# Kernel tuning notes

Measured on AMD Instinct MI355X. Metric: run time of the kernel, lower is better.

The kernel has to match this reference:

```python
import jax, jax.numpy as jnp
import numpy as np

N_NODES = 50000
N_EDGES = 800000
NUM_GRAPHS = 256
BN_EPS = 1e-5


def setup_inputs() -> dict:
    key = jax.random.key(0)
    ks = jax.random.split(key, 16)
    in_dim, hid, out_dim = 64, 128, 1
    s = lambda k, shape, fan: jax.random.normal(k, shape, jnp.float32) / np.sqrt(fan)
    inp = {
        'x': jax.random.normal(ks[0], (N_NODES, in_dim), jnp.float32),
        'edge_index': jax.random.randint(ks[1], (2, N_EDGES), 0, N_NODES, jnp.int64),
        'batch': jnp.sort(jax.random.randint(ks[2], (N_NODES,), 0, NUM_GRAPHS, jnp.int64)),
        # SAGEConv layer 0 (in_dim->hid): Wn aggregated-neighbor weight (with bias), Wr root weight
        'Wn0': s(ks[3], (in_dim, hid), in_dim), 'Wr0': s(ks[4], (in_dim, hid), in_dim), 'b0': jnp.zeros((hid,), jnp.float32),
        'Wn1': s(ks[5], (hid, hid), hid), 'Wr1': s(ks[6], (hid, hid), hid), 'b1': jnp.zeros((hid,), jnp.float32),
        'Wn2': s(ks[7], (hid, hid), hid), 'Wr2': s(ks[8], (hid, hid), hid), 'b2': jnp.zeros((hid,), jnp.float32),
        'gamma': jnp.ones((3, hid), jnp.float32), 'beta': jnp.zeros((3, hid), jnp.float32),
        'fc1_W': s(ks[9], (hid, hid // 2), hid), 'fc1_b': jnp.zeros((hid // 2,), jnp.float32),
        'fc2_W': s(ks[10], (hid // 2, out_dim), hid // 2), 'fc2_b': jnp.zeros((out_dim,), jnp.float32),
    }
    return inp


def _sage_mean(x, src, dst, inv_deg, Wn, Wr, b):
    # mean-aggregate neighbor features then linear: lin_l(mean_j x_j) + lin_r(x_i)
    agg = jax.ops.segment_sum(x[src], dst, num_segments=N_NODES) * inv_deg
    return agg @ Wn + x @ Wr + b


def _bn_relu(h, g, bta):
    mu = jnp.mean(h, axis=0)
    var = jnp.var(h, axis=0)
    return jax.nn.relu((h - mu) * jax.lax.rsqrt(var + BN_EPS) * g + bta)


def reference(x, edge_index, batch, Wn0, Wr0, b0, Wn1, Wr1, b1, Wn2, Wr2, b2,
              gamma, beta, fc1_W, fc1_b, fc2_W, fc2_b):
    src, dst = edge_index[0], edge_index[1]
    deg = jax.ops.segment_sum(jnp.ones((src.shape[0],), x.dtype), dst, num_segments=N_NODES)
    inv_deg = (1.0 / jnp.maximum(deg, 1.0))[:, None]  # [N,1]

    h = _bn_relu(_sage_mean(x, src, dst, inv_deg, Wn0, Wr0, b0), gamma[0], beta[0])
    h = _bn_relu(_sage_mean(h, src, dst, inv_deg, Wn1, Wr1, b1), gamma[1], beta[1])
    h = _bn_relu(_sage_mean(h, src, dst, inv_deg, Wn2, Wr2, b2), gamma[2], beta[2])

    # global mean pool over graphs
    pooled = jax.ops.segment_sum(h, batch, num_segments=NUM_GRAPHS)
    cnt = jax.ops.segment_sum(jnp.ones((h.shape[0],), h.dtype), batch, num_segments=NUM_GRAPHS)
    pooled = pooled / jnp.maximum(cnt, 1.0)[:, None]

    z = jax.nn.relu(pooled @ fc1_W + fc1_b)
    return jax.nn.sigmoid(z @ fc2_W + fc2_b)  # [NUM_GRAPHS, 1]
```

## Files before the change

kernel.cpp:

```cpp
#include <hip/hip_runtime.h>

#define N_NODES 50000
#define N_EDGES 800000
#define NUM_GRAPHS 256
#define HID 128
#define IN_DIM 64
#define BN_EPS 1e-5f
#define SPREAD 16
#define NB 196
#define BUCKET 256
#define SCHUNK 4096
#define NCHUNK 196
#define PX_BLKS 1563
#define W0_BLKS 8
#define W1_BLKS 16
#define GB_BLKS 196

typedef __attribute__((ext_vector_type(8))) short bf16x8;
typedef __attribute__((ext_vector_type(4))) float f32x4;

__device__ __forceinline__ float bf2f(unsigned short u){ union{unsigned i;float f;}c; c.i=((unsigned)u)<<16; return c.f; }
__device__ __forceinline__ float bflo(unsigned w){ union{unsigned i;float f;}c; c.i=w<<16; return c.f; }
__device__ __forceinline__ float bfhi(unsigned w){ union{unsigned i;float f;}c; c.i=w&0xFFFF0000u; return c.f; }
__device__ __forceinline__ unsigned short f2bf(float f){ union{float f;unsigned i;}c; c.f=f; unsigned r=c.i+0x7FFF+((c.i>>16)&1); return (unsigned short)(r>>16); }
__device__ __forceinline__ unsigned fpack(float a, float b){
  union{float f;unsigned i;}ca,cb; ca.f=a; cb.f=b;
  unsigned ra=((ca.i+0x7FFF+((ca.i>>16)&1))>>16)&0xFFFFu;
  unsigned rb=(cb.i+0x7FFF+((cb.i>>16)&1))&0xFFFF0000u;
  return ra|rb;
}
__device__ __forceinline__ void acc8(float* a, uint4 u){
  a[0]+=bflo(u.x); a[1]+=bfhi(u.x); a[2]+=bflo(u.y); a[3]+=bfhi(u.y);
  a[4]+=bflo(u.z); a[5]+=bfhi(u.z); a[6]+=bflo(u.w); a[7]+=bfhi(u.w);
}

__global__ __launch_bounds__(256) void k_hist(const int* __restrict__ dst, int* __restrict__ bcount){
  __shared__ int h[NB];
  int t = threadIdx.x;
  for(int i=t;i<NB;i+=256) h[i]=0;
  __syncthreads();
  int base = blockIdx.x*SCHUNK;
  int n = min(SCHUNK, N_EDGES-base);
  for(int v=t; v<n; v+=256) atomicAdd(&h[dst[base+v]>>8], 1);
  __syncthreads();
  for(int i=t;i<NB;i+=256) if(h[i]) atomicAdd(&bcount[i], h[i]);
}

__global__ __launch_bounds__(256) void k_scatter_pack(const int* __restrict__ src, const int* __restrict__ dst,
      const int* __restrict__ bcount, int* __restrict__ bfill, unsigned* __restrict__ pairs,
      const float* __restrict__ x, unsigned short* __restrict__ H0,
      const float* __restrict__ Wn0, const float* __restrict__ Wr0, unsigned short* __restrict__ Bp0,
      const float* __restrict__ Wn1, const float* __restrict__ Wr1, unsigned short* __restrict__ Bp1,
      const float* __restrict__ Wn2, const float* __restrict__ Wr2, unsigned short* __restrict__ Bp2,
      const int* __restrict__ batch, int* __restrict__ gstart){
  __shared__ int h[NB], lbase[NB], gbase[NB], cur[NB];
  __shared__ int sc[256];
  __shared__ unsigned staged[SCHUNK];
  int blk = blockIdx.x, t = threadIdx.x;
  if(blk < NCHUNK){
    for(int i=t;i<NB;i+=256) h[i]=0;
    __syncthreads();
    int base = blk*SCHUNK;
    int n = min(SCHUNK, N_EDGES-base);
    for(int v=t; v<n; v+=256) atomicAdd(&h[dst[base+v]>>8], 1);
    __syncthreads();
    int bc = (t<NB)? bcount[t] : 0;
    sc[t]=bc; __syncthreads();
    for(int off=1;off<256;off<<=1){ int u=(t>=off)?sc[t-off]:0; __syncthreads(); sc[t]+=u; __syncthreads(); }
    int bb_t = sc[t]-bc;
    __syncthreads();
    int hv = (t<NB)? h[t] : 0;
    sc[t]=hv; __syncthreads();
    for(int off=1;off<256;off<<=1){ int u=(t>=off)?sc[t-off]:0; __syncthreads(); sc[t]+=u; __syncthreads(); }
    if(t<NB){ lbase[t]=sc[t]-hv; cur[t]=0; if(hv) gbase[t] = bb_t + atomicAdd(&bfill[t], hv); }
    __syncthreads();
    for(int v=t; v<n; v+=256){
      int s = src[base+v], d = dst[base+v];
      int b = d>>8;
      int rr = atomicAdd(&cur[b], 1);
      staged[lbase[b]+rr] = (unsigned)s | ((unsigned)(d&255)<<16) | ((unsigned)b<<24);
    }
    __syncthreads();
    for(int i=t; i<n; i+=256){
      unsigned p = staged[i];
      int b = (int)(p>>24);
      pairs[gbase[b] + (i - lbase[b])] = p;
    }
  } else if(blk < NCHUNK+PX_BLKS){
    int tid = (blk-NCHUNK)*256 + t;
    if(tid < N_NODES*8){
      int row = tid>>3, q = tid&7;
      float4 a = ((const float4*)x)[(size_t)row*16 + q*2];
      float4 b = ((const float4*)x)[(size_t)row*16 + q*2 + 1];
      uint4 o;
      o.x = fpack(a.x,a.y); o.y = fpack(a.z,a.w);
      o.z = fpack(b.x,b.y); o.w = fpack(b.z,b.w);
      ((uint4*)H0)[(size_t)row*8 + q] = o;
    }
  } else if(blk < NCHUNK+PX_BLKS+W0_BLKS+2*W1_BLKS){
    const float *Wn, *Wr; unsigned short* Bp; int KH, base;
    if(blk < NCHUNK+PX_BLKS+W0_BLKS){ Wn=Wn0; Wr=Wr0; Bp=Bp0; KH=IN_DIM; base=NCHUNK+PX_BLKS; }
    else if(blk < NCHUNK+PX_BLKS+W0_BLKS+W1_BLKS){ Wn=Wn1; Wr=Wr1; Bp=Bp1; KH=HID; base=NCHUNK+PX_BLKS+W0_BLKS; }
    else { Wn=Wn2; Wr=Wr2; Bp=Bp2; KH=HID; base=NCHUNK+PX_BLKS+W0_BLKS+W1_BLKS; }
    int NKS = (2*KH)/32;
    int id = (blk-base)*256 + t;
    if(id < 8*NKS*64){
      int lane = id & 63;
      int ks = (id>>6) % NKS;
      int nt = (id>>6) / NKS;
      int quad = lane>>4, m = lane&15;
      int c = nt*16 + m;
      unsigned short v[8];
      #pragma unroll
      for(int j=0;j<8;j++){
        int k = ks*32 + quad*8 + j;
        float w = (k < KH) ? Wn[(size_t)k*HID + c] : Wr[(size_t)(k-KH)*HID + c];
        v[j] = f2bf(w);
      }
      uint4 o;
      o.x = ((unsigned)v[1]<<16)|v[0]; o.y = ((unsigned)v[3]<<16)|v[2];
      o.z = ((unsigned)v[5]<<16)|v[4]; o.w = ((unsigned)v[7]<<16)|v[6];
      ((uint4*)Bp)[id] = o;
    }
  } else {
    int id = (blk - (NCHUNK+PX_BLKS+W0_BLKS+2*W1_BLKS))*256 + t;
    if(id < N_NODES){
      int b = batch[id];
      if(id == 0){
        for(int g=0; g<=b; g++) gstart[g] = 0;
      } else {
        int pv = batch[id-1];
        if(pv != b) for(int g=pv+1; g<=b; g++) gstart[g] = id;
      }
      if(id == N_NODES-1){
        for(int g=b+1; g<=NUM_GRAPHS; g++) gstart[g] = N_NODES;
      }
    }
  }
}

__global__ __launch_bounds__(1024) void k_csr(const unsigned* __restrict__ pairs, const int* __restrict__ bcount,
                int* __restrict__ rowptr, float* __restrict__ invdeg, unsigned short* __restrict__ eidx){
  __shared__ int cnt[BUCKET], cur[BUCKET], sc[BUCKET];
  __shared__ int bb[2];
  int t = threadIdx.x;
  int b = blockIdx.x;
  if(t==0){ bb[0]=0; bb[1]=0; }
  if(t<BUCKET) cnt[t]=0;
  __syncthreads();
  if(t<NB){
    int c = bcount[t];
    if(t<b)  atomicAdd(&bb[0], c);
    if(t<=b) atomicAdd(&bb[1], c);
  }
  __syncthreads();
  int e0 = bb[0], e1 = bb[1];
  int node0 = b*BUCKET;
  for(int i=e0+t; i<e1; i+=1024) atomicAdd(&cnt[(int)((pairs[i]>>16)&0xFF)], 1);
  __syncthreads();
  if(t<BUCKET) sc[t]=cnt[t];
  __syncthreads();
  for(int off=1;off<BUCKET;off<<=1){
    int u=0;
    if(t<BUCKET && t>=off) u=sc[t-off];
    __syncthreads();
    if(t<BUCKET) sc[t]+=u;
    __syncthreads();
  }
  if(t<BUCKET && node0+t < N_NODES){
    int pre = sc[t]-cnt[t] + e0;
    rowptr[node0+t] = pre;
    cur[t] = pre;
    invdeg[node0+t] = 1.0f/(float)max(cnt[t],1);
  }
  if(b==0 && t==0) rowptr[N_NODES] = N_EDGES;
  __syncthreads();
  for(int i=e0+t; i<e1; i+=1024){
    unsigned p = pairs[i];
    int pos = atomicAdd(&cur[(p>>16)&0xFF], 1);
    eidx[pos] = (unsigned short)(p & 0xFFFF);
  }
}

template<int KH>
__global__ __launch_bounds__(256) void k_agg_gemm(const unsigned short* __restrict__ H,
                     const unsigned short* __restrict__ eidx, const int* __restrict__ rowptr,
                     const float* __restrict__ invdeg,
                     const unsigned short* __restrict__ Bp, const float* __restrict__ bias,
                     unsigned short* __restrict__ raw,
                     float* __restrict__ psum, float* __restrict__ psq){
  const int NKS = (2*KH)/32;
  const int LKS = KH/32;
  const int F8  = KH/8;
  const int SPL = 16/F8;
  const int LDA = KH + 4;
  const int EDGE_CAP = 512;
  __shared__ unsigned short Alds[16*LDA];
  __shared__ unsigned short Elds[EDGE_CAP];
  __shared__ int rp[17];
  int t = threadIdx.x;
  int wave = t>>6, lane = t&63;
  int row0b = blockIdx.x*16;

  if(t < 17) rp[t] = rowptr[row0b + t];
  __syncthreads();
  int ebase = rp[0];
  int etot  = rp[16] - ebase;
  bool fits = (etot <= EDGE_CAP);
  if(fits){
    for(int i=t; i<etot; i+=256) Elds[i] = eidx[ebase + i];
  }
  __syncthreads();

  int rr = lane >> 4;
  int h  = (SPL==1) ? 0 : ((lane>>3)&1);
  int q  = lane & (F8-1);
  int li = wave*4 + rr;
  int b = rp[li] - ebase, e = rp[li+1] - ebase;
  float acc[8] = {0,0,0,0,0,0,0,0};

#define LDH(s) (*(const uint4*)(H + (size_t)(s)*KH + q*8))
#define GBODY(FETCH) { \
    int i = b + h; \
    for(; i + 7*SPL < e; i += 8*SPL){ \
      int s0=FETCH(i), s1=FETCH(i+SPL), s2=FETCH(i+2*SPL), s3=FETCH(i+3*SPL), \
          s4=FETCH(i+4*SPL), s5=FETCH(i+5*SPL), s6=FETCH(i+6*SPL), s7=FETCH(i+7*SPL); \
      uint4 u0=LDH(s0),u1=LDH(s1),u2=LDH(s2),u3=LDH(s3),u4=LDH(s4),u5=LDH(s5),u6=LDH(s6),u7=LDH(s7); \
      acc8(acc,u0); acc8(acc,u1); acc8(acc,u2); acc8(acc,u3); \
      acc8(acc,u4); acc8(acc,u5); acc8(acc,u6); acc8(acc,u7); \
    } \
    for(; i + 3*SPL < e; i += 4*SPL){ \
      int s0=FETCH(i), s1=FETCH(i+SPL), s2=FETCH(i+2*SPL), s3=FETCH(i+3*SPL); \
      uint4 u0=LDH(s0),u1=LDH(s1),u2=LDH(s2),u3=LDH(s3); \
      acc8(acc,u0); acc8(acc,u1); acc8(acc,u2); acc8(acc,u3); \
    } \
    for(; i < e; i += SPL){ \
      int s0=FETCH(i); uint4 u0=LDH(s0); acc8(acc,u0); \
    } }
#define FL(i) ((int)Elds[(i)])
#define FG(i) ((int)eidx[ebase + (i)])
  if(fits){ GBODY(FL) } else { GBODY(FG) }
#undef FL
#undef FG
#undef GBODY
#undef LDH

  if(SPL==2){
    #pragma unroll
    for(int k=0;k<8;k++) acc[k] += __shfl_xor(acc[k], 8, 64);
  }
  if(h==0){
    float id = invdeg[row0b + li];
    uint4 o;
    o.x = fpack(acc[0]*id, acc[1]*id); o.y = fpack(acc[2]*id, acc[3]*id);
    o.z = fpack(acc[4]*id, acc[5]*id); o.w = fpack(acc[6]*id, acc[7]*id);
    *(uint4*)(Alds + li*LDA + q*8) = o;
  }
  __syncthreads();

  int m = lane&15, quad = lane>>4;
  const unsigned short* Arow = Alds + m*LDA + quad*8;
  const unsigned short* Hrow = H + (size_t)(row0b+m)*KH + quad*8;
  f32x4 facc[2];
  facc[0] = (f32x4){0.f,0.f,0.f,0.f};
  facc[1] = (f32x4){0.f,0.f,0.f,0.f};
  #pragma unroll 1
  for(int ks=0; ks<NKS; ks++){
    bf16x8 a = (ks < LKS) ? *(const bf16x8*)(Arow + ks*32)
                          : *(const bf16x8*)(Hrow + (size_t)(ks-LKS)*32);
    const unsigned short* bp = Bp + (((size_t)(wave*2)*NKS + ks)*64 + lane)*8;
    bf16x8 b0 = *(const bf16x8*)(bp);
    bf16x8 b1 = *(const bf16x8*)(bp + (size_t)NKS*64*8);
    facc[0] = __builtin_amdgcn_mfma_f32_16x16x32_bf16(a, b0, facc[0], 0, 0, 0);
    facc[1] = __builtin_amdgcn_mfma_f32_16x16x32_bf16(a, b1, facc[1], 0, 0, 0);
  }
  int sp = blockIdx.x & (SPREAD-1);
  #pragma unroll
  for(int nt=0;nt<2;nt++){
    int col = wave*32 + nt*16 + m;
    float bv = bias[col];
    float s = 0.f, s2 = 0.f;
    #pragma unroll
    for(int reg=0;reg<4;reg++){
      float v = facc[nt][reg] + bv;
      int row = row0b + quad*4 + reg;
      raw[(size_t)row*HID + col] = f2bf(v);
      s += v; s2 += v*v;
    }
    s  += __shfl_xor(s, 16, 64);  s  += __shfl_xor(s, 32, 64);
    s2 += __shfl_xor(s2, 16, 64); s2 += __shfl_xor(s2, 32, 64);
    if(quad==0){
      atomicAdd(&psum[sp*HID+col], s);
      atomicAdd(&psq [sp*HID+col], s2);
    }
  }
}

__global__ __launch_bounds__(256) void k_transform(const unsigned short* __restrict__ raw,
      const float* __restrict__ psum, const float* __restrict__ psq,
      const float* __restrict__ gamma, const float* __restrict__ beta,
      unsigned short* __restrict__ Hout){
  __shared__ float s_sc[HID], s_sf[HID];
  int t = threadIdx.x;
  if(t < HID){
    float s=0.f, s2=0.f;
    #pragma unroll
    for(int i=0;i<SPREAD;i++){ s += psum[i*HID+t]; s2 += psq[i*HID+t]; }
    float mu  = s  * (1.0f/(float)N_NODES);
    float var = s2 * (1.0f/(float)N_NODES) - mu*mu;
    float rstd = rsqrtf(var + BN_EPS);
    float sc = rstd * gamma[t];
    s_sc[t] = sc; s_sf[t] = beta[t] - mu*sc;
  }
  __syncthreads();
  int tid = blockIdx.x*256 + t;
  if(tid >= N_NODES*16) return;
  int q = tid & 15;
  uint4 u = ((const uint4*)raw)[tid];
  float f0 = fmaxf(fmaf(bflo(u.x), s_sc[q*8+0], s_sf[q*8+0]), 0.f);
  float f1 = fmaxf(fmaf(bfhi(u.x), s_sc[q*8+1], s_sf[q*8+1]), 0.f);
  float f2 = fmaxf(fmaf(bflo(u.y), s_sc[q*8+2], s_sf[q*8+2]), 0.f);
  float f3 = fmaxf(fmaf(bfhi(u.y), s_sc[q*8+3], s_sf[q*8+3]), 0.f);
  float f4 = fmaxf(fmaf(bflo(u.z), s_sc[q*8+4], s_sf[q*8+4]), 0.f);
  float f5 = fmaxf(fmaf(bfhi(u.z), s_sc[q*8+5], s_sf[q*8+5]), 0.f);
  float f6 = fmaxf(fmaf(bflo(u.w), s_sc[q*8+6], s_sf[q*8+6]), 0.f);
  float f7 = fmaxf(fmaf(bfhi(u.w), s_sc[q*8+7], s_sf[q*8+7]), 0.f);
  uint4 o;
  o.x = fpack(f0,f1); o.y = fpack(f2,f3); o.z = fpack(f4,f5); o.w = fpack(f6,f7);
  ((uint4*)Hout)[tid] = o;
}

__global__ __launch_bounds__(256) void k_poolmlp(const unsigned short* __restrict__ raw,
      const int* __restrict__ gstart,
      const float* __restrict__ psum, const float* __restrict__ psq,
      const float* __restrict__ gamma, const float* __restrict__ beta,
      const float* __restrict__ fc1W, const float* __restrict__ fc1b,
      const float* __restrict__ fc2W, const float* __restrict__ fc2b,
      float* __restrict__ out){
  __shared__ float s_sc[HID], s_sf[HID];
  __shared__ float red[16][HID];
  __shared__ float p[HID];
  int g = blockIdx.x, t = threadIdx.x;
  if(t < HID){
    float s=0.f, s2=0.f;
    #pragma unroll
    for(int i=0;i<SPREAD;i++){ s += psum[i*HID+t]; s2 += psq[i*HID+t]; }
    float mu  = s  * (1.0f/(float)N_NODES);
    float var = s2 * (1.0f/(float)N_NODES) - mu*mu;
    float rstd = rsqrtf(var + BN_EPS);
    float sc = rstd * gamma[t];
    s_sc[t] = sc; s_sf[t] = beta[t] - mu*sc;
  }
  __syncthreads();
  int r0 = gstart[g], r1 = gstart[g+1];
  int q = t & 15, rr = t >> 4;
  float acc[8] = {0,0,0,0,0,0,0,0};
  for(int n = r0 + rr; n < r1; n += 16){
    uint4 u = ((const uint4*)raw)[(size_t)n*16 + q];
    acc[0] += fmaxf(fmaf(bflo(u.x), s_sc[q*8+0], s_sf[q*8+0]), 0.f);
    acc[1] += fmaxf(fmaf(bfhi(u.x), s_sc[q*8+1], s_sf[q*8+1]), 0.f);
    acc[2] += fmaxf(fmaf(bflo(u.y), s_sc[q*8+2], s_sf[q*8+2]), 0.f);
    acc[3] += fmaxf(fmaf(bfhi(u.y), s_sc[q*8+3], s_sf[q*8+3]), 0.f);
    acc[4] += fmaxf(fmaf(bflo(u.z), s_sc[q*8+4], s_sf[q*8+4]), 0.f);
    acc[5] += fmaxf(fmaf(bfhi(u.z), s_sc[q*8+5], s_sf[q*8+5]), 0.f);
    acc[6] += fmaxf(fmaf(bflo(u.w), s_sc[q*8+6], s_sf[q*8+6]), 0.f);
    acc[7] += fmaxf(fmaf(bfhi(u.w), s_sc[q*8+7], s_sf[q*8+7]), 0.f);
  }
  #pragma unroll
  for(int k=0;k<8;k++) red[rr][q*8+k] = acc[k];
  __syncthreads();
  if(t < HID){
    float s = 0.f;
    #pragma unroll
    for(int j=0;j<16;j++) s += red[j][t];
    float ic = 1.0f / fmaxf((float)(r1 - r0), 1.0f);
    p[t] = s * ic;
  }
  __syncthreads();
  if(t < 64){
    float z = fc1b[t];
    #pragma unroll 4
    for(int k=0;k<HID;k++) z += p[k]*fc1W[k*64 + t];
    z = fmaxf(z, 0.f);
    float v = z * fc2W[t];
    #pragma unroll
    for(int off=32; off>0; off>>=1) v += __shfl_down(v, off, 64);
    if(t==0) out[g] = 1.0f/(1.0f + expf(-(v + fc2b[0])));
  }
}

extern "C" void kernel_launch(void* const* d_in, const int* in_sizes, int n_in,
                              void* d_out, int out_size, void* d_ws, size_t ws_size,
                              hipStream_t stream){
  const float* x    = (const float*)d_in[0];
  const int*   ei   = (const int*)d_in[1];
  const int*   batch= (const int*)d_in[2];
  const float* Wn0=(const float*)d_in[3]; const float* Wr0=(const float*)d_in[4]; const float* b0=(const float*)d_in[5];
  const float* Wn1=(const float*)d_in[6]; const float* Wr1=(const float*)d_in[7]; const float* b1=(const float*)d_in[8];
  const float* Wn2=(const float*)d_in[9]; const float* Wr2=(const float*)d_in[10]; const float* b2=(const float*)d_in[11];
  const float* gamma=(const float*)d_in[12]; const float* beta=(const float*)d_in[13];
  const float* fc1W=(const float*)d_in[14]; const float* fc1b=(const float*)d_in[15];
  const float* fc2W=(const float*)d_in[16]; const float* fc2b=(const float*)d_in[17];
  float* out = (float*)d_out;

  char* ws = (char*)d_ws;
  size_t off = 0;
  auto alloc = [&](size_t bytes)->char*{ char* p = ws + off; off += (bytes + 255) & ~(size_t)255; return p; };

  char* zero0   = ws + off;
  int*   bcount = (int*)alloc((size_t)NB*4);
  int*   bfill  = (int*)alloc((size_t)NB*4);
  float* pstats = (float*)alloc((size_t)3*2*SPREAD*HID*4);
  size_t zbytes = (size_t)((ws + off) - zero0);

  unsigned short* H0  = (unsigned short*)alloc((size_t)N_NODES*IN_DIM*2);
  unsigned short* H1  = (unsigned short*)alloc((size_t)N_NODES*HID*2);
  unsigned short* H2  = (unsigned short*)alloc((size_t)N_NODES*HID*2);
  unsigned short* raw = (unsigned short*)alloc((size_t)N_NODES*HID*2);
  unsigned short* Bp0 = (unsigned short*)alloc((size_t)8*4*64*8*2);
  unsigned short* Bp1 = (unsigned short*)alloc((size_t)8*8*64*8*2);
  unsigned short* Bp2 = (unsigned short*)alloc((size_t)8*8*64*8*2);
  float* invdeg = (float*)alloc((size_t)N_NODES*4);
  int* rowptr   = (int*)alloc((size_t)(N_NODES+1)*4);
  unsigned short* eidx = (unsigned short*)alloc((size_t)N_EDGES*2);
  unsigned* pairs = (unsigned*)alloc((size_t)N_EDGES*4);
  int* gstart   = (int*)alloc((size_t)(NUM_GRAPHS+1)*4);

  auto psumL = [&](int l){ return pstats + (size_t)l*2*SPREAD*HID; };
  auto psqL  = [&](int l){ return pstats + (size_t)l*2*SPREAD*HID + (size_t)SPREAD*HID; };

  const int* src = ei;
  const int* dst = ei + N_EDGES;

  hipMemsetAsync(zero0, 0, zbytes, stream);

  k_hist<<<NCHUNK, 256, 0, stream>>>(dst, bcount);
  k_scatter_pack<<<NCHUNK+PX_BLKS+W0_BLKS+2*W1_BLKS+GB_BLKS, 256, 0, stream>>>(src, dst, bcount, bfill, pairs,
      x, H0, Wn0, Wr0, Bp0, Wn1, Wr1, Bp1, Wn2, Wr2, Bp2, batch, gstart);
  k_csr<<<NB, 1024, 0, stream>>>(pairs, bcount, rowptr, invdeg, eidx);

  const int AG_BLKS = (N_NODES + 15)/16;

  k_agg_gemm<IN_DIM><<<AG_BLKS, 256, 0, stream>>>(H0, eidx, rowptr, invdeg, Bp0, b0, raw, psumL(0), psqL(0));
  k_transform<<<(N_NODES*16)/256, 256, 0, stream>>>(raw, psumL(0), psqL(0), gamma+0*HID, beta+0*HID, H1);
  k_agg_gemm<HID><<<AG_BLKS, 256, 0, stream>>>(H1, eidx, rowptr, invdeg, Bp1, b1, raw, psumL(1), psqL(1));
  k_transform<<<(N_NODES*16)/256, 256, 0, stream>>>(raw, psumL(1), psqL(1), gamma+1*HID, beta+1*HID, H2);
  k_agg_gemm<HID><<<AG_BLKS, 256, 0, stream>>>(H2, eidx, rowptr, invdeg, Bp2, b2, raw, psumL(2), psqL(2));

  k_poolmlp<<<NUM_GRAPHS, 256, 0, stream>>>(raw, gstart, psumL(2), psqL(2), gamma+2*HID, beta+2*HID,
      fc1W, fc1b, fc2W, fc2b, out);
}
```

Measured before the change: 264.0 us.

## Replace bucketed two-pass CSR build with global atomic degree count, scan, fill

Drops the bucket histogram, staged scatter into pairs, and per-bucket CSR kernel. Instead it builds CSR with a per-node global atomic degree count fused into the pack kernel, then a single-block scan over 50000 nodes, then an atomic-cursor fill of eidx. This removes the pairs buffer and one pass over the edges. In exchange it adds 800k global atomics on random addresses in two kernels and a serial single-block scan, and the order of neighbors within each row becomes nondeterministic.

```diff
diff --git a/kernel.cpp b/kernel.cpp
--- a/kernel.cpp
+++ b/kernel.cpp
@@ -7,10 +7,7 @@
 #define IN_DIM 64
 #define BN_EPS 1e-5f
 #define SPREAD 16
-#define NB 196
-#define BUCKET 256
-#define SCHUNK 4096
-#define NCHUNK 196
+#define DEG_BLKS 3125
 #define PX_BLKS 1563
 #define W0_BLKS 8
 #define W1_BLKS 16
@@ -34,60 +31,18 @@
   a[4]+=bflo(u.z); a[5]+=bfhi(u.z); a[6]+=bflo(u.w); a[7]+=bfhi(u.w);
 }
 
-__global__ __launch_bounds__(256) void k_hist(const int* __restrict__ dst, int* __restrict__ bcount){
-  __shared__ int h[NB];
-  int t = threadIdx.x;
-  for(int i=t;i<NB;i+=256) h[i]=0;
-  __syncthreads();
-  int base = blockIdx.x*SCHUNK;
-  int n = min(SCHUNK, N_EDGES-base);
-  for(int v=t; v<n; v+=256) atomicAdd(&h[dst[base+v]>>8], 1);
-  __syncthreads();
-  for(int i=t;i<NB;i+=256) if(h[i]) atomicAdd(&bcount[i], h[i]);
-}
-
-__global__ __launch_bounds__(256) void k_scatter_pack(const int* __restrict__ src, const int* __restrict__ dst,
-      const int* __restrict__ bcount, int* __restrict__ bfill, unsigned* __restrict__ pairs,
+__global__ __launch_bounds__(256) void k_degpack(const int* __restrict__ dst, int* __restrict__ deg,
       const float* __restrict__ x, unsigned short* __restrict__ H0,
       const float* __restrict__ Wn0, const float* __restrict__ Wr0, unsigned short* __restrict__ Bp0,
       const float* __restrict__ Wn1, const float* __restrict__ Wr1, unsigned short* __restrict__ Bp1,
       const float* __restrict__ Wn2, const float* __restrict__ Wr2, unsigned short* __restrict__ Bp2,
       const int* __restrict__ batch, int* __restrict__ gstart){
-  __shared__ int h[NB], lbase[NB], gbase[NB], cur[NB];
-  __shared__ int sc[256];
-  __shared__ unsigned staged[SCHUNK];
   int blk = blockIdx.x, t = threadIdx.x;
-  if(blk < NCHUNK){
-    for(int i=t;i<NB;i+=256) h[i]=0;
-    __syncthreads();
-    int base = blk*SCHUNK;
-    int n = min(SCHUNK, N_EDGES-base);
-    for(int v=t; v<n; v+=256) atomicAdd(&h[dst[base+v]>>8], 1);
-    __syncthreads();
-    int bc = (t<NB)? bcount[t] : 0;
-    sc[t]=bc; __syncthreads();
-    for(int off=1;off<256;off<<=1){ int u=(t>=off)?sc[t-off]:0; __syncthreads(); sc[t]+=u; __syncthreads(); }
-    int bb_t = sc[t]-bc;
-    __syncthreads();
-    int hv = (t<NB)? h[t] : 0;
-    sc[t]=hv; __syncthreads();
-    for(int off=1;off<256;off<<=1){ int u=(t>=off)?sc[t-off]:0; __syncthreads(); sc[t]+=u; __syncthreads(); }
-    if(t<NB){ lbase[t]=sc[t]-hv; cur[t]=0; if(hv) gbase[t] = bb_t + atomicAdd(&bfill[t], hv); }
-    __syncthreads();
-    for(int v=t; v<n; v+=256){
-      int s = src[base+v], d = dst[base+v];
-      int b = d>>8;
-      int rr = atomicAdd(&cur[b], 1);
-      staged[lbase[b]+rr] = (unsigned)s | ((unsigned)(d&255)<<16) | ((unsigned)b<<24);
-    }
-    __syncthreads();
-    for(int i=t; i<n; i+=256){
-      unsigned p = staged[i];
-      int b = (int)(p>>24);
-      pairs[gbase[b] + (i - lbase[b])] = p;
-    }
-  } else if(blk < NCHUNK+PX_BLKS){
-    int tid = (blk-NCHUNK)*256 + t;
+  if(blk < DEG_BLKS){
+    int i = blk*256 + t;
+    if(i < N_EDGES) atomicAdd(&deg[dst[i]], 1);
+  } else if(blk < DEG_BLKS+PX_BLKS){
+    int tid = (blk-DEG_BLKS)*256 + t;
     if(tid < N_NODES*8){
       int row = tid>>3, q = tid&7;
       float4 a = ((const float4*)x)[(size_t)row*16 + q*2];
@@ -97,11 +52,11 @@
       o.z = fpack(b.x,b.y); o.w = fpack(b.z,b.w);
       ((uint4*)H0)[(size_t)row*8 + q] = o;
     }
-  } else if(blk < NCHUNK+PX_BLKS+W0_BLKS+2*W1_BLKS){
+  } else if(blk < DEG_BLKS+PX_BLKS+W0_BLKS+2*W1_BLKS){
     const float *Wn, *Wr; unsigned short* Bp; int KH, base;
-    if(blk < NCHUNK+PX_BLKS+W0_BLKS){ Wn=Wn0; Wr=Wr0; Bp=Bp0; KH=IN_DIM; base=NCHUNK+PX_BLKS; }
-    else if(blk < NCHUNK+PX_BLKS+W0_BLKS+W1_BLKS){ Wn=Wn1; Wr=Wr1; Bp=Bp1; KH=HID; base=NCHUNK+PX_BLKS+W0_BLKS; }
-    else { Wn=Wn2; Wr=Wr2; Bp=Bp2; KH=HID; base=NCHUNK+PX_BLKS+W0_BLKS+W1_BLKS; }
+    if(blk < DEG_BLKS+PX_BLKS+W0_BLKS){ Wn=Wn0; Wr=Wr0; Bp=Bp0; KH=IN_DIM; base=DEG_BLKS+PX_BLKS; }
+    else if(blk < DEG_BLKS+PX_BLKS+W0_BLKS+W1_BLKS){ Wn=Wn1; Wr=Wr1; Bp=Bp1; KH=HID; base=DEG_BLKS+PX_BLKS+W0_BLKS; }
+    else { Wn=Wn2; Wr=Wr2; Bp=Bp2; KH=HID; base=DEG_BLKS+PX_BLKS+W0_BLKS+W1_BLKS; }
     int NKS = (2*KH)/32;
     int id = (blk-base)*256 + t;
     if(id < 8*NKS*64){
@@ -123,7 +78,7 @@
       ((uint4*)Bp)[id] = o;
     }
   } else {
-    int id = (blk - (NCHUNK+PX_BLKS+W0_BLKS+2*W1_BLKS))*256 + t;
+    int id = (blk - (DEG_BLKS+PX_BLKS+W0_BLKS+2*W1_BLKS))*256 + t;
     if(id < N_NODES){
       int b = batch[id];
       if(id == 0){
@@ -139,46 +94,41 @@
   }
 }
 
-__global__ __launch_bounds__(1024) void k_csr(const unsigned* __restrict__ pairs, const int* __restrict__ bcount,
-                int* __restrict__ rowptr, float* __restrict__ invdeg, unsigned short* __restrict__ eidx){
-  __shared__ int cnt[BUCKET], cur[BUCKET], sc[BUCKET];
-  __shared__ int bb[2];
+__global__ __launch_bounds__(1024) void k_scan(const int* __restrict__ deg,
+      int* __restrict__ rowptr, int* __restrict__ cur, float* __restrict__ invdeg){
+  __shared__ int part[1024];
+  const int PER = (N_NODES + 1023)/1024;
   int t = threadIdx.x;
-  int b = blockIdx.x;
-  if(t==0){ bb[0]=0; bb[1]=0; }
-  if(t<BUCKET) cnt[t]=0;
-  __syncthreads();
-  if(t<NB){
-    int c = bcount[t];
-    if(t<b)  atomicAdd(&bb[0], c);
-    if(t<=b) atomicAdd(&bb[1], c);
-  }
-  __syncthreads();
-  int e0 = bb[0], e1 = bb[1];
-  int node0 = b*BUCKET;
-  for(int i=e0+t; i<e1; i+=1024) atomicAdd(&cnt[(int)((pairs[i]>>16)&0xFF)], 1);
-  __syncthreads();
-  if(t<BUCKET) sc[t]=cnt[t];
-  __syncthreads();
-  for(int off=1;off<BUCKET;off<<=1){
-    int u=0;
-    if(t<BUCKET && t>=off) u=sc[t-off];
+  int base = t*PER;
+  int cnt = N_NODES - base; if(cnt < 0) cnt = 0; if(cnt > PER) cnt = PER;
+  int s = 0;
+  for(int j=0;j<cnt;j++) s += deg[base+j];
+  part[t] = s;
+  __syncthreads();
+  for(int off=1; off<1024; off<<=1){
+    int u = (t>=off)? part[t-off] : 0;
     __syncthreads();
-    if(t<BUCKET) sc[t]+=u;
+    part[t] += u;
     __syncthreads();
   }
-  if(t<BUCKET && node0+t < N_NODES){
-    int pre = sc[t]-cnt[t] + e0;
-    rowptr[node0+t] = pre;
-    cur[t] = pre;
-    invdeg[node0+t] = 1.0f/(float)max(cnt[t],1);
-  }
-  if(b==0 && t==0) rowptr[N_NODES] = N_EDGES;
-  __syncthreads();
-  for(int i=e0+t; i<e1; i+=1024){
-    unsigned p = pairs[i];
-    int pos = atomicAdd(&cur[(p>>16)&0xFF], 1);
-    eidx[pos] = (unsigned short)(p & 0xFFFF);
+  int run = part[t] - s;
+  for(int j=0;j<cnt;j++){
+    int d = deg[base+j];
+    rowptr[base+j] = run;
+    cur[base+j]    = run;
+    invdeg[base+j] = 1.0f/(float)max(d,1);
+    run += d;
+  }
+  if(t==0) rowptr[N_NODES] = N_EDGES;
+}
+
+__global__ __launch_bounds__(256) void k_fill(const int* __restrict__ src, const int* __restrict__ dst,
+      int* __restrict__ cur, unsigned short* __restrict__ eidx){
+  int i = blockIdx.x*256 + threadIdx.x;
+  if(i < N_EDGES){
+    int d = dst[i];
+    int pos = atomicAdd(&cur[d], 1);
+    eidx[pos] = (unsigned short)src[i];
   }
 }
 
@@ -408,8 +358,7 @@
   auto alloc = [&](size_t bytes)->char*{ char* p = ws + off; off += (bytes + 255) & ~(size_t)255; return p; };
 
   char* zero0   = ws + off;
-  int*   bcount = (int*)alloc((size_t)NB*4);
-  int*   bfill  = (int*)alloc((size_t)NB*4);
+  int*   deg    = (int*)alloc((size_t)N_NODES*4);
   float* pstats = (float*)alloc((size_t)3*2*SPREAD*HID*4);
   size_t zbytes = (size_t)((ws + off) - zero0);
 
@@ -422,8 +371,8 @@
   unsigned short* Bp2 = (unsigned short*)alloc((size_t)8*8*64*8*2);
   float* invdeg = (float*)alloc((size_t)N_NODES*4);
   int* rowptr   = (int*)alloc((size_t)(N_NODES+1)*4);
+  int* cur      = (int*)alloc((size_t)N_NODES*4);
   unsigned short* eidx = (unsigned short*)alloc((size_t)N_EDGES*2);
-  unsigned* pairs = (unsigned*)alloc((size_t)N_EDGES*4);
   int* gstart   = (int*)alloc((size_t)(NUM_GRAPHS+1)*4);
 
   auto psumL = [&](int l){ return pstats + (size_t)l*2*SPREAD*HID; };
@@ -434,10 +383,10 @@
 
   hipMemsetAsync(zero0, 0, zbytes, stream);
 
-  k_hist<<<NCHUNK, 256, 0, stream>>>(dst, bcount);
-  k_scatter_pack<<<NCHUNK+PX_BLKS+W0_BLKS+2*W1_BLKS+GB_BLKS, 256, 0, stream>>>(src, dst, bcount, bfill, pairs,
+  k_degpack<<<DEG_BLKS+PX_BLKS+W0_BLKS+2*W1_BLKS+GB_BLKS, 256, 0, stream>>>(dst, deg,
       x, H0, Wn0, Wr0, Bp0, Wn1, Wr1, Bp1, Wn2, Wr2, Bp2, batch, gstart);
-  k_csr<<<NB, 1024, 0, stream>>>(pairs, bcount, rowptr, invdeg, eidx);
+  k_scan<<<1, 1024, 0, stream>>>(deg, rowptr, cur, invdeg);
+  k_fill<<<DEG_BLKS, 256, 0, stream>>>(src, dst, cur, eidx);
 
   const int AG_BLKS = (N_NODES + 15)/16;
 
```

Measured after the change: 441.1 us. 1.67x slower.
